# Performance work log

Hardware: AMD Instinct MI355X
Metric: run time of the kernel (lower is better)

Reference implementation:

```python
import jax, jax.numpy as jnp
import numpy as np

D_MODEL = 2048
D_STATE = 16
BATCH = 2048

def setup_inputs() -> dict:
    key = jax.random.key(0)
    ks = jax.random.split(key, 8)
    x_t = jax.random.normal(ks[0], (BATCH, D_MODEL), dtype=jnp.float32)
    ssm_state_prev = jax.random.normal(ks[1], (BATCH, D_MODEL, D_STATE), dtype=jnp.float32)
    # parameters (match torch init semantics loosely; values random)
    A_log = jnp.log(jnp.tile(jnp.arange(1, D_STATE + 1, dtype=jnp.float32)[None, :], (D_MODEL, 1)))
    s = 1.0 / np.sqrt(D_MODEL)
    W_B = jax.random.uniform(ks[2], (D_STATE, D_MODEL), minval=-s, maxval=s, dtype=jnp.float32)
    W_C = jax.random.uniform(ks[3], (D_STATE, D_MODEL), minval=-s, maxval=s, dtype=jnp.float32)
    W_Delta = jax.random.uniform(ks[4], (D_MODEL, D_MODEL), minval=-s, maxval=s, dtype=jnp.float32)
    b_Delta = jax.random.uniform(ks[5], (D_MODEL,), minval=-s, maxval=s, dtype=jnp.float32)
    D_param = jnp.ones((D_MODEL,), dtype=jnp.float32)
    return {"x_t": x_t, "ssm_state_prev": ssm_state_prev, "A_log": A_log,
            "W_B": W_B, "W_C": W_C, "W_Delta": W_Delta, "b_Delta": b_Delta,
            "D_param": D_param}

def reference(x_t, ssm_state_prev, A_log, W_B, W_C, W_Delta, b_Delta, D_param):
    A = -jnp.exp(A_log)                         # (d_model, d_state)
    B_t = x_t @ W_B.T                            # (B, d_state)
    C_t = x_t @ W_C.T                            # (B, d_state)
    Delta_t = jax.nn.softplus(x_t @ W_Delta.T + b_Delta)   # (B, d_model)
    A_bar = jnp.exp(Delta_t[:, :, None] * A[None, :, :])   # (B, d_model, d_state)
    Delta_B = Delta_t[:, :, None] * B_t[:, None, :]         # (B, d_model, d_state)
    ssm_state_t = A_bar * ssm_state_prev + Delta_B * x_t[:, :, None]
    y_t = jnp.sum(ssm_state_t * C_t[:, None, :], axis=-1) + D_param * x_t
    return (y_t, ssm_state_t)
```

## Files before the change

### kernel.cpp

```cpp
#include <hip/hip_runtime.h>

#define D_MODEL 2048
#define D_STATE 16
#define BATCH   2048

typedef __attribute__((ext_vector_type(8))) short bf16x8;
typedef __attribute__((ext_vector_type(4))) float f32x4;
typedef __attribute__((ext_vector_type(8))) unsigned short u16x8;

__device__ __forceinline__ unsigned short f2bf(float f) {
  unsigned u = __float_as_uint(f);
  u = (u + 0x7FFFu + ((u >> 16) & 1u)) >> 16;
  return (unsigned short)u;
}

__device__ __forceinline__ void cvt8(const float* __restrict__ s, unsigned short* __restrict__ d) {
  f32x4 a = *(const f32x4*)s;
  f32x4 b = *(const f32x4*)(s + 4);
  u16x8 o;
  o[0] = f2bf(a[0]); o[1] = f2bf(a[1]); o[2] = f2bf(a[2]); o[3] = f2bf(a[3]);
  o[4] = f2bf(b[0]); o[5] = f2bf(b[1]); o[6] = f2bf(b[2]); o[7] = f2bf(b[3]);
  *(u16x8*)d = o;
}

__global__ __launch_bounds__(256) void prep_kernel(
    const float* __restrict__ x, const float* __restrict__ wd,
    const float* __restrict__ wb, const float* __restrict__ wc,
    const float* __restrict__ alog,
    unsigned short* __restrict__ x_bf, unsigned short* __restrict__ w_bf,
    unsigned short* __restrict__ wbc, float* __restrict__ nA) {
  int t = blockIdx.x * 256 + threadIdx.x;
  if (t < 524288) {
    cvt8(x + t * 8, x_bf + t * 8);
  } else if (t < 1048576) {
    int i = (t - 524288) * 8;
    cvt8(wd + i, w_bf + i);
  } else if (t < 1081344) {
    int i = (t - 1048576) * 8;
    int row = i >> 11, col = i & 2047;
    if (row < 16)      cvt8(wb + row * 2048 + col, wbc + i);
    else if (row < 32) cvt8(wc + (row - 16) * 2048 + col, wbc + i);
    else { u16x8 z = {0,0,0,0,0,0,0,0}; *(u16x8*)(wbc + i) = z; }
  } else {
    int i = (t - 1081344) * 4;
    f32x4 v = *(const f32x4*)(alog + i);
    f32x4 o;
    o[0] = __expf(v[0]); o[1] = __expf(v[1]); o[2] = __expf(v[2]); o[3] = __expf(v[3]);
    *(f32x4*)(nA + i) = o;
  }
}

__global__ __launch_bounds__(256) void gemm_kernel(
    const unsigned short* __restrict__ Abf,
    const unsigned short* __restrict__ Wbf,
    const unsigned short* __restrict__ WBC,
    const float* __restrict__ bias,
    float* __restrict__ Delta,
    float* __restrict__ BC) {
  __shared__ __align__(16) unsigned short lA[2][8192];
  __shared__ __align__(16) unsigned short lB[2][8192];

  const int tid = threadIdx.x;
  const bool isBC = (blockIdx.y == 16);
  const int brow = blockIdx.x * 128;
  const int bcol = isBC ? 0 : blockIdx.y * 128;
  const unsigned short* Bsrc = isBC ? WBC : (Wbf + (size_t)bcol * 2048);
  const unsigned short* Asrc = Abf + (size_t)brow * 2048;

  const int lane = tid & 63;
  const int wid = tid >> 6;
  const int wr = wid >> 1, wcid = wid & 1;
  const int fr = lane & 15;
  const int kg = lane >> 4;

  int srcoff[4];
#pragma unroll
  for (int i = 0; i < 4; ++i) {
    int ci = i * 256 + tid;
    int r = ci >> 3, cs = ci & 7;
    int c = cs ^ (r & 7);
    srcoff[i] = r * 2048 + c * 8;
  }
  const int ldsb = (tid >> 6) << 10;

  f32x4 acc[4][4];
#pragma unroll
  for (int m = 0; m < 4; ++m)
#pragma unroll
    for (int n = 0; n < 4; ++n) acc[m][n] = (f32x4){0.f, 0.f, 0.f, 0.f};

#define STAGE(buf, k0)                                                          \
  do {                                                                          \
    _Pragma("unroll")                                                           \
    for (int i = 0; i < 4; ++i)                                                 \
      __builtin_amdgcn_global_load_lds(                                         \
          (const __attribute__((address_space(1))) void*)(Asrc + (size_t)srcoff[i] + (k0)), \
          (__attribute__((address_space(3))) void*)((char*)lA[buf] + i * 4096 + ldsb), \
          16, 0, 0);                                                            \
    _Pragma("unroll")                                                           \
    for (int i = 0; i < 4; ++i)                                                 \
      __builtin_amdgcn_global_load_lds(                                         \
          (const __attribute__((address_space(1))) void*)(Bsrc + (size_t)srcoff[i] + (k0)), \
          (__attribute__((address_space(3))) void*)((char*)lB[buf] + i * 4096 + ldsb), \
          16, 0, 0);                                                            \
  } while (0)

  STAGE(0, 0);
  asm volatile("s_waitcnt vmcnt(0)" ::: "memory");
  __builtin_amdgcn_s_barrier();
  int cur = 0;
#pragma unroll 1
  for (int t = 0; t < 32; ++t) {
    if (t < 31) STAGE(cur ^ 1, (t + 1) * 64);

    bf16x8 fa[2][4], fb[2][4];
#pragma unroll
    for (int m = 0; m < 4; ++m) {
      int row = wr * 64 + m * 16 + fr;
#pragma unroll
      for (int kk = 0; kk < 2; ++kk)
        fa[kk][m] = *(const bf16x8*)((const char*)lA[cur] + row * 128 +
                                     ((((kk << 2) + kg) ^ (row & 7)) << 4));
    }
#pragma unroll
    for (int n = 0; n < 4; ++n) {
      int row = wcid * 64 + n * 16 + fr;
#pragma unroll
      for (int kk = 0; kk < 2; ++kk)
        fb[kk][n] = *(const bf16x8*)((const char*)lB[cur] + row * 128 +
                                     ((((kk << 2) + kg) ^ (row & 7)) << 4));
    }
#pragma unroll
    for (int kk = 0; kk < 2; ++kk)
#pragma unroll
      for (int m = 0; m < 4; ++m)
#pragma unroll
        for (int n = 0; n < 4; ++n)
          acc[m][n] = __builtin_amdgcn_mfma_f32_16x16x32_bf16(fa[kk][m], fb[kk][n], acc[m][n], 0, 0, 0);

    asm volatile("s_waitcnt vmcnt(0)" ::: "memory");
    __builtin_amdgcn_s_barrier();
    cur ^= 1;
  }
#undef STAGE

  const int rq = kg * 4;
#pragma unroll
  for (int m = 0; m < 4; ++m) {
    int grow = brow + wr * 64 + m * 16 + rq;
#pragma unroll
    for (int n = 0; n < 4; ++n) {
      int gcol = bcol + wcid * 64 + n * 16 + fr;
      if (!isBC) {
        float bv = bias[gcol];
#pragma unroll
        for (int q = 0; q < 4; ++q) {
          float v = acc[m][n][q] + bv;
          v = fmaxf(v, 0.f) + log1pf(__expf(-fabsf(v)));
          Delta[(size_t)(grow + q) * 2048 + gcol] = v;
        }
      } else {
#pragma unroll
        for (int q = 0; q < 4; ++q)
          BC[(size_t)(grow + q) * 128 + gcol] = acc[m][n][q];
      }
    }
  }
}

__global__ __launch_bounds__(256) void pointwise_kernel(
    const float* __restrict__ x, const float* __restrict__ sp,
    const float* __restrict__ nA, const float* __restrict__ BCb,
    const float* __restrict__ Delta, const float* __restrict__ Dp,
    float* __restrict__ y, float* __restrict__ st) {
  int t = blockIdx.x * 256 + threadIdx.x;
  int sg = t & 1;
  int d = (t >> 1) & 2047;
  int b = t >> 12;
  int bd = (b << 11) + d;
  float delta = Delta[bd];
  float xv = x[bd];
  float dx = delta * xv;
  const f32x4* spp = (const f32x4*)sp + ((size_t)t << 1);
  f32x4 s0 = __builtin_nontemporal_load(spp);
  f32x4 s1 = __builtin_nontemporal_load(spp + 1);
  const f32x4* ap = (const f32x4*)nA + ((d << 2) + (sg << 1));
  f32x4 a0 = ap[0], a1 = ap[1];
  const f32x4* bp = (const f32x4*)BCb + ((b << 5) + (sg << 1));
  f32x4 b0 = bp[0], b1 = bp[1];
  f32x4 c0 = bp[4], c1 = bp[5];
  f32x4 r0, r1;
  r0[0] = __expf(-delta * a0[0]) * s0[0] + dx * b0[0];
  r0[1] = __expf(-delta * a0[1]) * s0[1] + dx * b0[1];
  r0[2] = __expf(-delta * a0[2]) * s0[2] + dx * b0[2];
  r0[3] = __expf(-delta * a0[3]) * s0[3] + dx * b0[3];
  r1[0] = __expf(-delta * a1[0]) * s1[0] + dx * b1[0];
  r1[1] = __expf(-delta * a1[1]) * s1[1] + dx * b1[1];
  r1[2] = __expf(-delta * a1[2]) * s1[2] + dx * b1[2];
  r1[3] = __expf(-delta * a1[3]) * s1[3] + dx * b1[3];
  f32x4* stp = (f32x4*)st + ((size_t)t << 1);
  stp[0] = r0;
  stp[1] = r1;
  float p = r0[0] * c0[0] + r0[1] * c0[1] + r0[2] * c0[2] + r0[3] * c0[3]
          + r1[0] * c1[0] + r1[1] * c1[1] + r1[2] * c1[2] + r1[3] * c1[3];
  p += __shfl_xor(p, 1, 2);
  if (sg == 0) y[bd] = p + Dp[d] * xv;
}

extern "C" void kernel_launch(void* const* d_in, const int* in_sizes, int n_in,
                              void* d_out, int out_size, void* d_ws, size_t ws_size,
                              hipStream_t stream) {
  const float* x    = (const float*)d_in[0];
  const float* sp   = (const float*)d_in[1];
  const float* alog = (const float*)d_in[2];
  const float* wb   = (const float*)d_in[3];
  const float* wc   = (const float*)d_in[4];
  const float* wd   = (const float*)d_in[5];
  const float* bdel = (const float*)d_in[6];
  const float* dp   = (const float*)d_in[7];
  float* y  = (float*)d_out;
  float* st = (float*)d_out + (size_t)BATCH * D_MODEL;

  char* ws = (char*)d_ws;
  unsigned short* x_bf = (unsigned short*)ws;
  unsigned short* w_bf = (unsigned short*)(ws + 8388608);
  unsigned short* wbc  = (unsigned short*)(ws + 16777216);
  float* Delta = (float*)(ws + 17301504);
  float* BC    = (float*)(ws + 34078720);
  float* nA    = (float*)(ws + 35127296);

  prep_kernel<<<4256, 256, 0, stream>>>(x, wd, wb, wc, alog, x_bf, w_bf, wbc, nA);
  gemm_kernel<<<dim3(16, 17), 256, 0, stream>>>(x_bf, w_bf, wbc, bdel, Delta, BC);
  pointwise_kernel<<<32768, 256, 0, stream>>>(x, sp, nA, BC, Delta, dp, y, st);
}
```

Before: 550.9 us.

## Split GEMM K dimension in two and reduce partials in pointwise kernel

The GEMM grid gains a z dimension of 2, and each block now covers half of K (1024). Each half writes raw partial sums to its own Delta and BC buffer. Bias add, softplus, and summing the two partials move into the pointwise kernel. The aim is to double the GEMM block count from 272 to 544 so the GPU's CUs are better filled, at the cost of an extra 16MB Delta partial written and read back, plus extra BC reads.

Result: no change. 555.1 us (+0.8%).

```diff
diff --git a/kernel.cpp b/kernel.cpp
--- a/kernel.cpp
+++ b/kernel.cpp
@@ -54,18 +54,21 @@
     const unsigned short* __restrict__ Abf,
     const unsigned short* __restrict__ Wbf,
     const unsigned short* __restrict__ WBC,
-    const float* __restrict__ bias,
-    float* __restrict__ Delta,
-    float* __restrict__ BC) {
+    float* __restrict__ Delta0, float* __restrict__ Delta1,
+    float* __restrict__ BC0, float* __restrict__ BC1) {
   __shared__ __align__(16) unsigned short lA[2][8192];
   __shared__ __align__(16) unsigned short lB[2][8192];
 
   const int tid = threadIdx.x;
   const bool isBC = (blockIdx.y == 16);
+  const int kz = blockIdx.z;
+  const int kbase = kz << 10;
   const int brow = blockIdx.x * 128;
   const int bcol = isBC ? 0 : blockIdx.y * 128;
   const unsigned short* Bsrc = isBC ? WBC : (Wbf + (size_t)bcol * 2048);
   const unsigned short* Asrc = Abf + (size_t)brow * 2048;
+  float* Dout = kz ? Delta1 : Delta0;
+  float* Bout = kz ? BC1 : BC0;
 
   const int lane = tid & 63;
   const int wid = tid >> 6;
@@ -105,13 +108,13 @@
           16, 0, 0);                                                            \
   } while (0)
 
-  STAGE(0, 0);
+  STAGE(0, kbase);
   asm volatile("s_waitcnt vmcnt(0)" ::: "memory");
   __builtin_amdgcn_s_barrier();
   int cur = 0;
 #pragma unroll 1
-  for (int t = 0; t < 32; ++t) {
-    if (t < 31) STAGE(cur ^ 1, (t + 1) * 64);
+  for (int t = 0; t < 16; ++t) {
+    if (t < 15) STAGE(cur ^ 1, kbase + (t + 1) * 64);
 
     bf16x8 fa[2][4], fb[2][4];
 #pragma unroll
@@ -152,17 +155,13 @@
     for (int n = 0; n < 4; ++n) {
       int gcol = bcol + wcid * 64 + n * 16 + fr;
       if (!isBC) {
-        float bv = bias[gcol];
-#pragma unroll
-        for (int q = 0; q < 4; ++q) {
-          float v = acc[m][n][q] + bv;
-          v = fmaxf(v, 0.f) + log1pf(__expf(-fabsf(v)));
-          Delta[(size_t)(grow + q) * 2048 + gcol] = v;
-        }
+#pragma unroll
+        for (int q = 0; q < 4; ++q)
+          Dout[(size_t)(grow + q) * 2048 + gcol] = acc[m][n][q];
       } else {
 #pragma unroll
         for (int q = 0; q < 4; ++q)
-          BC[(size_t)(grow + q) * 128 + gcol] = acc[m][n][q];
+          Bout[(size_t)(grow + q) * 128 + gcol] = acc[m][n][q];
       }
     }
   }
@@ -170,15 +169,18 @@
 
 __global__ __launch_bounds__(256) void pointwise_kernel(
     const float* __restrict__ x, const float* __restrict__ sp,
-    const float* __restrict__ nA, const float* __restrict__ BCb,
-    const float* __restrict__ Delta, const float* __restrict__ Dp,
+    const float* __restrict__ nA, const float* __restrict__ BC0,
+    const float* __restrict__ BC1,
+    const float* __restrict__ Delta0, const float* __restrict__ Delta1,
+    const float* __restrict__ bias, const float* __restrict__ Dp,
     float* __restrict__ y, float* __restrict__ st) {
   int t = blockIdx.x * 256 + threadIdx.x;
   int sg = t & 1;
   int d = (t >> 1) & 2047;
   int b = t >> 12;
   int bd = (b << 11) + d;
-  float delta = Delta[bd];
+  float dpre = Delta0[bd] + Delta1[bd] + bias[d];
+  float delta = fmaxf(dpre, 0.f) + log1pf(__expf(-fabsf(dpre)));
   float xv = x[bd];
   float dx = delta * xv;
   const f32x4* spp = (const f32x4*)sp + ((size_t)t << 1);
@@ -186,9 +188,10 @@
   f32x4 s1 = __builtin_nontemporal_load(spp + 1);
   const f32x4* ap = (const f32x4*)nA + ((d << 2) + (sg << 1));
   f32x4 a0 = ap[0], a1 = ap[1];
-  const f32x4* bp = (const f32x4*)BCb + ((b << 5) + (sg << 1));
-  f32x4 b0 = bp[0], b1 = bp[1];
-  f32x4 c0 = bp[4], c1 = bp[5];
+  const f32x4* bp0 = (const f32x4*)BC0 + ((b << 5) + (sg << 1));
+  const f32x4* bp1 = (const f32x4*)BC1 + ((b << 5) + (sg << 1));
+  f32x4 b0 = bp0[0] + bp1[0], b1 = bp0[1] + bp1[1];
+  f32x4 c0 = bp0[4] + bp1[4], c1 = bp0[5] + bp1[5];
   f32x4 r0, r1;
   r0[0] = __expf(-delta * a0[0]) * s0[0] + dx * b0[0];
   r0[1] = __expf(-delta * a0[1]) * s0[1] + dx * b0[1];
@@ -225,11 +228,13 @@
   unsigned short* x_bf = (unsigned short*)ws;
   unsigned short* w_bf = (unsigned short*)(ws + 8388608);
   unsigned short* wbc  = (unsigned short*)(ws + 16777216);
-  float* Delta = (float*)(ws + 17301504);
-  float* BC    = (float*)(ws + 34078720);
-  float* nA    = (float*)(ws + 35127296);
+  float* nA     = (float*)(ws + 17301504);
+  float* Delta0 = (float*)(ws + 17432576);
+  float* Delta1 = (float*)(ws + 34209792);
+  float* BC0    = (float*)(ws + 50987008);
+  float* BC1    = (float*)(ws + 52035584);
 
   prep_kernel<<<4256, 256, 0, stream>>>(x, wd, wb, wc, alog, x_bf, w_bf, wbc, nA);
-  gemm_kernel<<<dim3(16, 17), 256, 0, stream>>>(x_bf, w_bf, wbc, bdel, Delta, BC);
-  pointwise_kernel<<<32768, 256, 0, stream>>>(x, sp, nA, BC, Delta, dp, y, st);
-}
+  gemm_kernel<<<dim3(16, 17, 2), 256, 0, stream>>>(x_bf, w_bf, wbc, Delta0, Delta1, BC0, BC1);
+  pointwise_kernel<<<32768, 256, 0, stream>>>(x, sp, nA, BC0, BC1, Delta0, Delta1, bdel, dp, y, st);
+}
```
